# Optimization experiments

Measured on AMD Instinct MI355X. Metric: run time of the kernel, lower is better.

## Reference

```python
import jax, jax.numpy as jnp
import numpy as np

B, N, M, C, H, W = 8, 16, 4, 2, 256, 256
GAMMA = 0.5   # gamma0
BETA = 1.0    # beta
EPS = 1e-8


def setup_inputs() -> dict:
    key = jax.random.key(0)
    k1, k2, k3, k4 = jax.random.split(key, 4)
    gt_arr = jax.random.randint(k1, (B, M, H, W), 0, C)
    sample_arr = jax.random.uniform(k2, (B, N, C, H, W), dtype=jnp.float32)
    prob = jax.random.uniform(k3, (B, N), dtype=jnp.float32)
    prob_gt = jax.random.uniform(k4, (B, M), dtype=jnp.float32)
    prob_gt = prob_gt / prob_gt.sum(-1, keepdims=True)  # gt mixture weights sum to 1
    sample_shape = jnp.array([4, 4], dtype=jnp.int64 if jax.config.read('jax_enable_x64') else jnp.int32)  # (K,S); unused since G0=1
    return {"gt_arr": gt_arr, "sample_arr": sample_arr, "prob": prob,
            "prob_gt": prob_gt, "sample_shape": sample_shape}


def _cost_iou(sample, gt_oh):
    # sample: (B,N,C,HW), gt_oh: (B,M,C,HW) -> cost (B,N,M)
    inter = jnp.einsum('bnch,bmch->bnmc', sample, gt_oh)
    union = sample.sum(-1)[:, :, None, :] + gt_oh.sum(-1)[:, None, :, :] - inter
    # drop background channel 0, mean over remaining channels
    return 1.0 - ((inter + 1.0) / (union + 1.0))[..., 1:].mean(-1)


def _coupling(cost, prob_gt):
    # Greedy sequential OT coupling (gamma != 1 branch), vectorized per gt column
    # via water-filling over cost-sorted samples; sequential over gt columns.
    Bn, Nn, Mn = cost.shape
    mass = 1.0 / Mn

    def per_batch(cb):  # cb: (N,M)
        order_gt = jnp.argsort(cb.min(axis=0))  # gts by their min cost

        def step(carry, i):
            rowsums, P = carry
            col = cb[:, i]                      # (N,)
            ordj = jnp.argsort(col)             # samples by cost for this gt
            caps = GAMMA - rowsums[ordj]        # remaining capacity, >= 0
            excl = jnp.cumsum(caps) - caps      # exclusive prefix of capacities
            a_sorted = jnp.clip(mass - excl, 0.0, caps)
            assign = jnp.zeros((Nn,), cb.dtype).at[ordj].set(a_sorted)
            P = P.at[:, i].set(assign)
            return (rowsums + assign, P), None

        init = (jnp.zeros((Nn,), cb.dtype), jnp.zeros((Nn, Mn), cb.dtype))
        (_, P), _ = jax.lax.scan(step, init, order_gt)
        return P

    P = jax.vmap(per_batch)(cost)
    return P * (prob_gt * Mn)[:, None, :]


def _forward(gt_arr, sample_arr, prob, prob_gt):
    Bn, Nn, Cn, Hn, Wn = sample_arr.shape
    Mn = gt_arr.shape[1]
    sample = sample_arr.reshape(Bn, Nn, Cn, Hn * Wn)
    gt_oh = jnp.transpose(
        jax.nn.one_hot(gt_arr.reshape(Bn, Mn, Hn * Wn), Cn, dtype=sample.dtype),
        (0, 1, 3, 2))                            # (B,M,C,HW)
    cost = _cost_iou(sample, gt_oh)              # (B,N,M)
    P = jax.lax.stop_gradient(_coupling(jax.lax.stop_gradient(cost), prob_gt))
    seg_loss = (P * cost).sum((1, 2)).mean()
    # KL: F.kl_div(log(prob+eps), target_prob) with 'mean' reduction (xlogy at 0)
    target = P.sum(-1)                           # (B,N)
    logp = jnp.log(prob + EPS)
    safe_t = jnp.where(target > 0, target, 1.0)
    kl = jnp.where(target > 0, target * (jnp.log(safe_t) - logp), 0.0).mean()
    loss = seg_loss + BETA * kl
    return loss, seg_loss, kl


def reference(gt_arr, sample_arr, prob, prob_gt, sample_shape):
    return _forward(gt_arr, sample_arr, prob, prob_gt)
```

## Files before the change

kernel.cpp:

```cpp
#include <hip/hip_runtime.h>
#include <math.h>

static constexpr int Bn = 8;
static constexpr int Nn = 16;
static constexpr int Mn = 4;
static constexpr int Cn = 2;
static constexpr int HWn = 256 * 256;
static constexpr int SEGS = 64;
static constexpr int SEGLEN = HWn / SEGS;
#define GAMMA_F 0.5f
#define MASS_F 0.25f
#define EPS_F 1e-8f


__global__ __launch_bounds__(256) void inter_kernel(
    const float* __restrict__ sample, const int* __restrict__ gt,
    float* __restrict__ accum) {
  int seg = blockIdx.x & (SEGS - 1);
  int b = blockIdx.x >> 6;
  int tid = threadIdx.x;
  int w = tid >> 6;
  int lane = tid & 63;
  size_t segoff = (size_t)seg * SEGLEN;

  const int* gtb = gt + ((size_t)b * Mn) * HWn + segoff;
  const float* sb = sample + (size_t)b * Nn * Cn * HWn + HWn + segoff;

  float ss[4] = {0.f, 0.f, 0.f, 0.f};
  float im[4][4] = {};
  float cnt[4] = {0.f, 0.f, 0.f, 0.f};

#pragma unroll
  for (int q = 0; q < 4; ++q) {
    int idx = q * 64 + lane;
    int4 g0 = reinterpret_cast<const int4*>(gtb + 0 * HWn)[idx];
    int4 g1 = reinterpret_cast<const int4*>(gtb + 1 * HWn)[idx];
    int4 g2 = reinterpret_cast<const int4*>(gtb + 2 * HWn)[idx];
    int4 g3 = reinterpret_cast<const int4*>(gtb + 3 * HWn)[idx];
    float mf[4][4];
    {
      int a0[4] = {g0.x, g0.y, g0.z, g0.w};
      int a1[4] = {g1.x, g1.y, g1.z, g1.w};
      int a2[4] = {g2.x, g2.y, g2.z, g2.w};
      int a3[4] = {g3.x, g3.y, g3.z, g3.w};
#pragma unroll
      for (int e = 0; e < 4; ++e) {
        mf[e][0] = (a0[e] == 1) ? 1.f : 0.f;
        mf[e][1] = (a1[e] == 1) ? 1.f : 0.f;
        mf[e][2] = (a2[e] == 1) ? 1.f : 0.f;
        mf[e][3] = (a3[e] == 1) ? 1.f : 0.f;
      }
    }
#pragma unroll
    for (int m = 0; m < 4; ++m)
      cnt[m] += (mf[0][m] + mf[1][m]) + (mf[2][m] + mf[3][m]);
#pragma unroll
    for (int nn = 0; nn < 4; ++nn) {
      const float* spn = sb + (size_t)(w * 4 + nn) * (Cn * HWn);
      float4 x = reinterpret_cast<const float4*>(spn)[idx];
      float xs[4] = {x.x, x.y, x.z, x.w};
#pragma unroll
      for (int e = 0; e < 4; ++e) {
        float v = xs[e];
        ss[nn] += v;
#pragma unroll
        for (int m = 0; m < 4; ++m) im[nn][m] = fmaf(v, mf[e][m], im[nn][m]);
      }
    }
  }

  __shared__ __align__(16) float red[4][20][68];
  __shared__ __align__(16) float redc[4][68];
#pragma unroll
  for (int nn = 0; nn < 4; ++nn) {
    red[w][nn * 5 + 0][lane] = ss[nn];
#pragma unroll
    for (int m = 0; m < 4; ++m) red[w][nn * 5 + 1 + m][lane] = im[nn][m];
  }
  if (w == 0) {
#pragma unroll
    for (int m = 0; m < 4; ++m) redc[m][lane] = cnt[m];
  }
  __syncthreads();

  if (tid < 80) {
    int rw = tid / 20, v = tid % 20;
    const float4* row = reinterpret_cast<const float4*>(&red[rw][v][0]);
    float4 a4 = row[0];
#pragma unroll
    for (int j = 1; j < 16; ++j) {
      float4 t = row[j];
      a4.x += t.x; a4.y += t.y; a4.z += t.z; a4.w += t.w;
    }
    float s = (a4.x + a4.y) + (a4.z + a4.w);
    int n = rw * 4 + v / 5;
    int k = v % 5;
    int bn = b * Nn + n;
    float* dst = (k == 0) ? (accum + 512 + bn) : (accum + bn * Mn + (k - 1));
    atomicAdd(dst, s);
  } else if (tid < 84) {
    int m = tid - 80;
    const float4* row = reinterpret_cast<const float4*>(&redc[m][0]);
    float4 a4 = row[0];
#pragma unroll
    for (int j = 1; j < 16; ++j) {
      float4 t = row[j];
      a4.x += t.x; a4.y += t.y; a4.z += t.z; a4.w += t.w;
    }
    float s = (a4.x + a4.y) + (a4.z + a4.w);
    atomicAdd(accum + 640 + b * Mn + m, s);
  }
}

__global__ __launch_bounds__(256) void finish_kernel(
    const float* __restrict__ accum,
    const float* __restrict__ prob, const float* __restrict__ prob_gt,
    float* __restrict__ out) {
  __shared__ __align__(16) float s_cost[Bn * Nn * Mn];
  __shared__ float s_red[8];
  int tid = threadIdx.x;

  if (tid < Bn * Nn) {
    float4 im = reinterpret_cast<const float4*>(accum)[tid];
    float sv = accum[512 + tid];
    int b = tid >> 4;
    float4 g = reinterpret_cast<const float4*>(accum + 640)[b];
    float4 c;
    c.x = 1.0f - (im.x + 1.0f) / (sv + g.x - im.x + 1.0f);
    c.y = 1.0f - (im.y + 1.0f) / (sv + g.y - im.y + 1.0f);
    c.z = 1.0f - (im.z + 1.0f) / (sv + g.z - im.z + 1.0f);
    c.w = 1.0f - (im.w + 1.0f) / (sv + g.w - im.w + 1.0f);
    *reinterpret_cast<float4*>(&s_cost[tid * Mn]) = c;
  }
  __syncthreads();

  float seg_part = 0.f, kl_part = 0.f;
  if (tid < Bn * Nn) {
    int bb = tid >> 4;
    int n = tid & 15;
    int base = (tid & 63) & ~15;

    float4 cv = *reinterpret_cast<const float4*>(&s_cost[tid * Mn]);
    float cc0 = cv.x, cc1 = cv.y, cc2 = cv.z, cc3 = cv.w;
    float pg0 = prob_gt[bb * Mn + 0], pg1 = prob_gt[bb * Mn + 1];
    float pg2 = prob_gt[bb * Mn + 2], pg3 = prob_gt[bb * Mn + 3];

    float m0 = cc0, m1 = cc1, m2 = cc2, m3 = cc3;
#pragma unroll
    for (int off = 1; off < 16; off <<= 1) {
      m0 = fminf(m0, __shfl_xor(m0, off));
      m1 = fminf(m1, __shfl_xor(m1, off));
      m2 = fminf(m2, __shfl_xor(m2, off));
      m3 = fminf(m3, __shfl_xor(m3, off));
    }
    int r0 = (m1 < m0) + (m2 < m0) + (m3 < m0);
    int r1 = (m0 <= m1) + (m2 < m1) + (m3 < m1);
    int r2 = (m0 <= m2) + (m1 <= m2) + (m3 < m2);
    int r3 = (m0 <= m3) + (m1 <= m3) + (m2 <= m3);

    float rowsum = 0.f;
    float target = 0.f;
#pragma unroll
    for (int k = 0; k < Mn; ++k) {
      int i = (r0 == k) ? 0 : (r1 == k) ? 1 : (r2 == k) ? 2 : 3;
      float v = (i == 0) ? cc0 : (i == 1) ? cc1 : (i == 2) ? cc2 : cc3;
      float pg = (i == 0) ? pg0 : (i == 1) ? pg1 : (i == 2) ? pg2 : pg3;
      float cap = GAMMA_F - rowsum;
      float excl = 0.f;
#pragma unroll 4
      for (int j = 0; j < Nn; ++j) {
        float vj = __shfl(v, base + j);
        float capj = __shfl(cap, base + j);
        bool pred = (vj < v) || (vj == v && j < n);
        excl += pred ? capj : 0.f;
      }
      float a = fminf(fmaxf(MASS_F - excl, 0.f), cap);
      rowsum += a;
      float p = a * pg * (float)Mn;
      seg_part += p * v;
      target += p;
    }
    kl_part = (target > 0.f)
                  ? target * (logf(target) - logf(prob[tid] + EPS_F))
                  : 0.f;
  }

#pragma unroll
  for (int off = 32; off > 0; off >>= 1) {
    seg_part += __shfl_down(seg_part, off);
    kl_part += __shfl_down(kl_part, off);
  }
  int lane = tid & 63, wv = tid >> 6;
  if (lane == 0) { s_red[wv * 2] = seg_part; s_red[wv * 2 + 1] = kl_part; }
  __syncthreads();
  if (tid == 0) {
    float seg = 0.f, kl = 0.f;
    for (int q = 0; q < 4; ++q) { seg += s_red[q * 2]; kl += s_red[q * 2 + 1]; }
    seg /= (float)Bn;
    kl /= (float)(Bn * Nn);
    out[0] = seg + 1.0f * kl;
    out[1] = seg;
    out[2] = kl;
  }
}

extern "C" void kernel_launch(void* const* d_in, const int* in_sizes, int n_in,
                              void* d_out, int out_size, void* d_ws, size_t ws_size,
                              hipStream_t stream) {
  const int* gt = (const int*)d_in[0];
  const float* sample = (const float*)d_in[1];
  const float* prob = (const float*)d_in[2];
  const float* prob_gt = (const float*)d_in[3];
  float* out = (float*)d_out;
  float* accum = (float*)d_ws;

  hipMemsetAsync(accum, 0, 672 * sizeof(float), stream);
  inter_kernel<<<Bn * SEGS, 256, 0, stream>>>(sample, gt, accum);
  finish_kernel<<<1, 256, 0, stream>>>(accum, prob, prob_gt, out);
}
```

Before: 23.96 us.

## Fuse finish step into reduction kernel via last-block counter, double segment count

Merges the single-block finish kernel into the reduction kernel. Each block increments a global counter after its atomics, and the last block to arrive computes the IoU cost, the greedy coupling and the KL loss. Reads of the accumulators in that block use agent-scope atomic loads. This removes one kernel launch and the gap between the two dependent kernels. It also doubles the number of segments, so there are more, smaller blocks to spread the memory-bound pass across CUs. The one-hot compare becomes a plain int-to-float cast, which is valid only because labels are 0 or 1 when C=2. The cost is a serial tail on one block and extra atomic traffic on the counter.

```diff
diff --git a/kernel.cpp b/kernel.cpp
--- a/kernel.cpp
+++ b/kernel.cpp
@@ -6,18 +6,25 @@
 static constexpr int Mn = 4;
 static constexpr int Cn = 2;
 static constexpr int HWn = 256 * 256;
-static constexpr int SEGS = 64;
+static constexpr int SEGS = 128;
 static constexpr int SEGLEN = HWn / SEGS;
+static constexpr int GRID = Bn * SEGS;
 #define GAMMA_F 0.5f
 #define MASS_F 0.25f
 #define EPS_F 1e-8f
 
 
-__global__ __launch_bounds__(256) void inter_kernel(
+__device__ __forceinline__ float agent_load(const float* p) {
+  return __hip_atomic_load(p, __ATOMIC_RELAXED, __HIP_MEMORY_SCOPE_AGENT);
+}
+
+__global__ __launch_bounds__(256) void fused_kernel(
     const float* __restrict__ sample, const int* __restrict__ gt,
-    float* __restrict__ accum) {
+    const float* __restrict__ prob, const float* __restrict__ prob_gt,
+    float* __restrict__ accum, unsigned int* __restrict__ counter,
+    float* __restrict__ out) {
   int seg = blockIdx.x & (SEGS - 1);
-  int b = blockIdx.x >> 6;
+  int b = blockIdx.x >> 7;
   int tid = threadIdx.x;
   int w = tid >> 6;
   int lane = tid & 63;
@@ -26,12 +33,18 @@
   const int* gtb = gt + ((size_t)b * Mn) * HWn + segoff;
   const float* sb = sample + (size_t)b * Nn * Cn * HWn + HWn + segoff;
 
+  __shared__ __align__(16) float red[4][20][68];
+  __shared__ __align__(16) float redc[4][68];
+  __shared__ unsigned int s_last;
+  __shared__ __align__(16) float s_cost[Bn * Nn * Mn];
+  __shared__ float s_red[8];
+
   float ss[4] = {0.f, 0.f, 0.f, 0.f};
   float im[4][4] = {};
   float cnt[4] = {0.f, 0.f, 0.f, 0.f};
 
 #pragma unroll
-  for (int q = 0; q < 4; ++q) {
+  for (int q = 0; q < 2; ++q) {
     int idx = q * 64 + lane;
     int4 g0 = reinterpret_cast<const int4*>(gtb + 0 * HWn)[idx];
     int4 g1 = reinterpret_cast<const int4*>(gtb + 1 * HWn)[idx];
@@ -45,10 +58,10 @@
       int a3[4] = {g3.x, g3.y, g3.z, g3.w};
 #pragma unroll
       for (int e = 0; e < 4; ++e) {
-        mf[e][0] = (a0[e] == 1) ? 1.f : 0.f;
-        mf[e][1] = (a1[e] == 1) ? 1.f : 0.f;
-        mf[e][2] = (a2[e] == 1) ? 1.f : 0.f;
-        mf[e][3] = (a3[e] == 1) ? 1.f : 0.f;
+        mf[e][0] = (float)a0[e];
+        mf[e][1] = (float)a1[e];
+        mf[e][2] = (float)a2[e];
+        mf[e][3] = (float)a3[e];
       }
     }
 #pragma unroll
@@ -69,8 +82,6 @@
     }
   }
 
-  __shared__ __align__(16) float red[4][20][68];
-  __shared__ __align__(16) float redc[4][68];
 #pragma unroll
   for (int nn = 0; nn < 4; ++nn) {
     red[w][nn * 5 + 0][lane] = ss[nn];
@@ -110,26 +121,32 @@
     float s = (a4.x + a4.y) + (a4.z + a4.w);
     atomicAdd(accum + 640 + b * Mn + m, s);
   }
-}
-
-__global__ __launch_bounds__(256) void finish_kernel(
-    const float* __restrict__ accum,
-    const float* __restrict__ prob, const float* __restrict__ prob_gt,
-    float* __restrict__ out) {
-  __shared__ __align__(16) float s_cost[Bn * Nn * Mn];
-  __shared__ float s_red[8];
-  int tid = threadIdx.x;
+
+  asm volatile("s_waitcnt vmcnt(0)" ::: "memory");
+  __syncthreads();
+  if (tid == 0) {
+    unsigned int old = atomicAdd(counter, 1u);
+    s_last = (old == (unsigned int)(GRID - 1)) ? 1u : 0u;
+  }
+  __syncthreads();
+  if (s_last == 0u) return;
 
   if (tid < Bn * Nn) {
-    float4 im = reinterpret_cast<const float4*>(accum)[tid];
-    float sv = accum[512 + tid];
-    int b = tid >> 4;
-    float4 g = reinterpret_cast<const float4*>(accum + 640)[b];
+    float i0 = agent_load(accum + tid * Mn + 0);
+    float i1 = agent_load(accum + tid * Mn + 1);
+    float i2 = agent_load(accum + tid * Mn + 2);
+    float i3 = agent_load(accum + tid * Mn + 3);
+    float sv = agent_load(accum + 512 + tid);
+    int bb = tid >> 4;
+    float g0 = agent_load(accum + 640 + bb * Mn + 0);
+    float g1 = agent_load(accum + 640 + bb * Mn + 1);
+    float g2 = agent_load(accum + 640 + bb * Mn + 2);
+    float g3 = agent_load(accum + 640 + bb * Mn + 3);
     float4 c;
-    c.x = 1.0f - (im.x + 1.0f) / (sv + g.x - im.x + 1.0f);
-    c.y = 1.0f - (im.y + 1.0f) / (sv + g.y - im.y + 1.0f);
-    c.z = 1.0f - (im.z + 1.0f) / (sv + g.z - im.z + 1.0f);
-    c.w = 1.0f - (im.w + 1.0f) / (sv + g.w - im.w + 1.0f);
+    c.x = 1.0f - (i0 + 1.0f) / (sv + g0 - i0 + 1.0f);
+    c.y = 1.0f - (i1 + 1.0f) / (sv + g1 - i1 + 1.0f);
+    c.z = 1.0f - (i2 + 1.0f) / (sv + g2 - i2 + 1.0f);
+    c.w = 1.0f - (i3 + 1.0f) / (sv + g3 - i3 + 1.0f);
     *reinterpret_cast<float4*>(&s_cost[tid * Mn]) = c;
   }
   __syncthreads();
@@ -190,8 +207,7 @@
     seg_part += __shfl_down(seg_part, off);
     kl_part += __shfl_down(kl_part, off);
   }
-  int lane = tid & 63, wv = tid >> 6;
-  if (lane == 0) { s_red[wv * 2] = seg_part; s_red[wv * 2 + 1] = kl_part; }
+  if (lane == 0) { s_red[w * 2] = seg_part; s_red[w * 2 + 1] = kl_part; }
   __syncthreads();
   if (tid == 0) {
     float seg = 0.f, kl = 0.f;
@@ -212,9 +228,12 @@
   const float* prob = (const float*)d_in[2];
   const float* prob_gt = (const float*)d_in[3];
   float* out = (float*)d_out;
-  float* accum = (float*)d_ws;
-
-  hipMemsetAsync(accum, 0, 672 * sizeof(float), stream);
-  inter_kernel<<<Bn * SEGS, 256, 0, stream>>>(sample, gt, accum);
-  finish_kernel<<<1, 256, 0, stream>>>(accum, prob, prob_gt, out);
+
+  char* ws = (char*)d_ws;
+  float* accum = (float*)(ws + 0);
+  unsigned int* counter = (unsigned int*)(ws + 2688);
+
+  hipMemsetAsync(ws, 0, 2692, stream);
+  fused_kernel<<<GRID, 256, 0, stream>>>(sample, gt, prob, prob_gt,
+                                         accum, counter, out);
 }
```

Result: slower. 38.63 us (+61.2%).
